# Optimization experiments

Hardware: AMD Instinct MI355X
Metric: run time of the kernel (lower is better)

The kernel has to match this reference:

```python
import jax, jax.numpy as jnp
import numpy as np

N_NODES = 100000
N_EDGES = 3200000
D = 128


def setup_inputs() -> dict:
    key = jax.random.key(0)
    ks = jax.random.split(key, 6)
    x = jax.random.normal(ks[0], (N_NODES, D), dtype=jnp.float32)
    w = jax.random.uniform(ks[1], (N_EDGES,), dtype=jnp.float32)
    W = jax.random.normal(ks[2], (D, D), dtype=jnp.float32) * (1.0 / np.sqrt(D))
    b = jax.random.normal(ks[3], (D,), dtype=jnp.float32) * 0.01
    src = jax.random.randint(ks[4], (N_EDGES,), 0, N_NODES, dtype=jnp.int64)
    dst = jax.random.randint(ks[5], (N_EDGES,), 0, N_NODES, dtype=jnp.int64)
    return {"x": x, "w": w, "W": W, "b": b, "src": src, "dst": dst}


def reference(x, w, W, b, src, dst):
    # h = linear(x)  -> [N, D]
    h = x @ W.T + b
    # u_mul_e: gather source features, scale by per-edge weight  -> [E, D]
    m = h[src] * w[:, None]
    # sum aggregation at destinations (SpMM scatter-add)  -> [N, D]
    out = jax.ops.segment_sum(m, dst, num_segments=N_NODES)
    return out
```

## Files before the change

kernel.cpp:

```cpp
#include <hip/hip_runtime.h>
#include <hip/hip_fp16.h>

constexpr int N_NODES = 100000;
constexpr int N_EDGES = 3200000;
constexpr int NB2 = (N_NODES + 63) >> 6;
constexpr int LCAP = 2432;
constexpr int TILE2 = 12500;
constexpr int NTILE2 = N_EDGES / TILE2;
constexpr int NWIN = 8;
constexpr int NKEY = 64 * NWIN;

__global__ __launch_bounds__(256) void cvt_kernel(const float* __restrict__ x,
                                                  __half* __restrict__ xh) {
  const int stride = gridDim.x * 256;
  const int total = N_NODES * 128 / 4;
  for (int i = blockIdx.x * 256 + threadIdx.x; i < total; i += stride) {
    float4 v = ((const float4*)x)[i];
    ((__half2*)xh)[2 * i] = __floats2half2_rn(v.x, v.y);
    ((__half2*)xh)[2 * i + 1] = __floats2half2_rn(v.z, v.w);
  }
}

__global__ __launch_bounds__(1024) void bin5_kernel(
    const int* __restrict__ src, const int* __restrict__ dst,
    const float* __restrict__ w, int* __restrict__ gtail,
    int2* __restrict__ lists) {
  __shared__ int2 rec[TILE2];
  __shared__ unsigned short lid[TILE2];
  __shared__ int lcnt[NB2];
  __shared__ int loff[NB2];
  __shared__ int lbase[NB2];
  __shared__ int wsum[16];
  const int t = threadIdx.x;
  const int e0 = blockIdx.x * TILE2;

  for (int i = t; i < NB2; i += 1024) lcnt[i] = 0;
  __syncthreads();

  for (int i = t; i < TILE2; i += 1024)
    atomicAdd(&lcnt[dst[e0 + i] >> 6], 1);
  __syncthreads();

  {
    int i0 = 2 * t, i1 = 2 * t + 1;
    int c0 = (i0 < NB2) ? lcnt[i0] : 0;
    int c1 = (i1 < NB2) ? lcnt[i1] : 0;
    int v = c0 + c1;
    int inc = v;
    #pragma unroll
    for (int d = 1; d < 64; d <<= 1) {
      int u = __shfl_up(inc, d, 64);
      if ((t & 63) >= d) inc += u;
    }
    if ((t & 63) == 63) wsum[t >> 6] = inc;
    __syncthreads();
    if (t < 16) {
      int s = wsum[t];
      int inc2 = s;
      #pragma unroll
      for (int d = 1; d < 16; d <<= 1) {
        int u = __shfl_up(inc2, d, 64);
        if (t >= d) inc2 += u;
      }
      wsum[t] = inc2 - s;
    }
    __syncthreads();
    int excl = (inc - v) + wsum[t >> 6];
    if (i0 < NB2) loff[i0] = excl;
    if (i1 < NB2) loff[i1] = excl + c0;
  }
  __syncthreads();

  for (int i = t; i < NB2; i += 1024) {
    int c = lcnt[i];
    lbase[i] = (c > 0) ? atomicAdd(&gtail[i], c) : 0;
  }
  __syncthreads();
  for (int i = t; i < NB2; i += 1024) lcnt[i] = loff[i];
  __syncthreads();

  for (int i = t; i < TILE2; i += 1024) {
    int e = e0 + i;
    int d = dst[e];
    int l = d >> 6;
    int p = atomicAdd(&lcnt[l], 1);
    rec[p] = make_int2(src[e] | ((d & 63) << 17), __float_as_int(w[e]));
    lid[p] = (unsigned short)l;
  }
  __syncthreads();

  for (int q = t; q < TILE2; q += 1024) {
    int l = lid[q];
    int dest = lbase[l] + (q - loff[l]);
    if ((unsigned)dest < (unsigned)LCAP)
      lists[(size_t)l * LCAP + dest] = rec[q];
  }
}

__global__ __launch_bounds__(256) void agg6_kernel(
    const __half* __restrict__ xh, const int2* __restrict__ lists,
    const int* __restrict__ gtail, float* __restrict__ agg_out,
    float* __restrict__ sw) {
  __shared__ int2 sorted[LCAP];
  __shared__ int kcnt[NKEY];
  __shared__ int koff[NKEY + 1];
  __shared__ int kcur[NKEY];
  const int b = blockIdx.x;
  const int t = threadIdx.x;
  const int c = min(gtail[b], LCAP);
  const int2* base = lists + (size_t)b * LCAP;

  for (int i = t; i < NKEY; i += 256) kcnt[i] = 0;
  __syncthreads();

  for (int j = t; j < c; j += 256) {
    int rx = base[j].x;
    int key = ((rx >> 17) & 63) * 8 + ((rx & 0x1FFFF) >> 14);
    atomicAdd(&kcnt[key], 1);
  }
  __syncthreads();

  if (t < 64) {
    int base8 = t * 8;
    int loc[8], run = 0;
    #pragma unroll
    for (int i = 0; i < 8; ++i) { loc[i] = run; run += kcnt[base8 + i]; }
    int inc = run;
    #pragma unroll
    for (int d = 1; d < 64; d <<= 1) {
      int u = __shfl_up(inc, d, 64);
      if (t >= d) inc += u;
    }
    int excl = inc - run;
    #pragma unroll
    for (int i = 0; i < 8; ++i) {
      koff[base8 + i] = excl + loc[i];
      kcur[base8 + i] = excl + loc[i];
    }
    if (t == 63) koff[NKEY] = inc;
  }
  __syncthreads();

  for (int j = t; j < c; j += 256) {
    int2 r = base[j];
    int key = ((r.x >> 17) & 63) * 8 + ((r.x & 0x1FFFF) >> 14);
    int p = atomicAdd(&kcur[key], 1);
    if ((unsigned)p < (unsigned)LCAP) sorted[p] = r;
  }
  __syncthreads();

  const int wv = t >> 6, lane = t & 63;
  const int nd = min(64, N_NODES - b * 64);
  const __half2* xh2 = (const __half2*)xh;
  for (int ri = 0; ri < 16; ++ri) {
    int r = wv * 16 + ri;
    int j0 = min(koff[r * 8], c), j1 = min(koff[r * 8 + 8], c);
    float2 acc = make_float2(0.f, 0.f);
    float sws = 0.f;
    int j = j0;
    for (; j + 8 <= j1; j += 8) {
      int2 e0 = sorted[j];
      int2 e1 = sorted[j + 1];
      int2 e2 = sorted[j + 2];
      int2 e3 = sorted[j + 3];
      int2 e4 = sorted[j + 4];
      int2 e5 = sorted[j + 5];
      int2 e6 = sorted[j + 6];
      int2 e7 = sorted[j + 7];
      float2 v0 = __half22float2(xh2[(size_t)(e0.x & 0x1FFFF) * 64 + lane]);
      float2 v1 = __half22float2(xh2[(size_t)(e1.x & 0x1FFFF) * 64 + lane]);
      float2 v2 = __half22float2(xh2[(size_t)(e2.x & 0x1FFFF) * 64 + lane]);
      float2 v3 = __half22float2(xh2[(size_t)(e3.x & 0x1FFFF) * 64 + lane]);
      float2 v4 = __half22float2(xh2[(size_t)(e4.x & 0x1FFFF) * 64 + lane]);
      float2 v5 = __half22float2(xh2[(size_t)(e5.x & 0x1FFFF) * 64 + lane]);
      float2 v6 = __half22float2(xh2[(size_t)(e6.x & 0x1FFFF) * 64 + lane]);
      float2 v7 = __half22float2(xh2[(size_t)(e7.x & 0x1FFFF) * 64 + lane]);
      float w0 = __int_as_float(e0.y), w1 = __int_as_float(e1.y);
      float w2 = __int_as_float(e2.y), w3 = __int_as_float(e3.y);
      float w4 = __int_as_float(e4.y), w5 = __int_as_float(e5.y);
      float w6 = __int_as_float(e6.y), w7 = __int_as_float(e7.y);
      acc.x = fmaf(w0, v0.x, acc.x); acc.y = fmaf(w0, v0.y, acc.y);
      acc.x = fmaf(w1, v1.x, acc.x); acc.y = fmaf(w1, v1.y, acc.y);
      acc.x = fmaf(w2, v2.x, acc.x); acc.y = fmaf(w2, v2.y, acc.y);
      acc.x = fmaf(w3, v3.x, acc.x); acc.y = fmaf(w3, v3.y, acc.y);
      acc.x = fmaf(w4, v4.x, acc.x); acc.y = fmaf(w4, v4.y, acc.y);
      acc.x = fmaf(w5, v5.x, acc.x); acc.y = fmaf(w5, v5.y, acc.y);
      acc.x = fmaf(w6, v6.x, acc.x); acc.y = fmaf(w6, v6.y, acc.y);
      acc.x = fmaf(w7, v7.x, acc.x); acc.y = fmaf(w7, v7.y, acc.y);
      sws += ((w0 + w1) + (w2 + w3)) + ((w4 + w5) + (w6 + w7));
    }
    for (; j < j1; ++j) {
      int2 e0 = sorted[j];
      float2 v0 = __half22float2(xh2[(size_t)(e0.x & 0x1FFFF) * 64 + lane]);
      float w0 = __int_as_float(e0.y);
      acc.x = fmaf(w0, v0.x, acc.x);
      acc.y = fmaf(w0, v0.y, acc.y);
      sws += w0;
    }
    if (r < nd) {
      ((float2*)agg_out)[(size_t)(b * 64 + r) * 64 + lane] = acc;
      if (lane == 0) sw[b * 64 + r] = sws;
    }
  }
}

__global__ __launch_bounds__(256, 2) void linear3_kernel(
    float* __restrict__ io, const float* __restrict__ W,
    const float* __restrict__ bias, const float* __restrict__ sw) {
  __shared__ float Wt[128][132];
  const int t = threadIdx.x;
  const int row0 = blockIdx.x * 64;

  #pragma unroll
  for (int i = 0; i < 16; ++i) {
    int f4 = t + 256 * i;
    int c = f4 >> 5;
    int k = (f4 & 31) * 4;
    float4 v = *(const float4*)(W + (size_t)c * 128 + k);
    Wt[k + 0][c] = v.x;
    Wt[k + 1][c] = v.y;
    Wt[k + 2][c] = v.z;
    Wt[k + 3][c] = v.w;
  }
  __syncthreads();

  const int tx = t & 15;
  const int ty = t >> 4;
  const float* xr[4];
  #pragma unroll
  for (int i = 0; i < 4; ++i) {
    int r = row0 + ty * 4 + i;
    xr[i] = (r < N_NODES) ? (io + (size_t)r * 128) : io;
  }

  float acc[4][8];
  #pragma unroll
  for (int i = 0; i < 4; ++i)
    #pragma unroll
    for (int j = 0; j < 8; ++j) acc[i][j] = 0.f;

  for (int k0 = 0; k0 < 128; k0 += 4) {
    float4 a[4];
    #pragma unroll
    for (int i = 0; i < 4; ++i) a[i] = *(const float4*)(xr[i] + k0);
    #pragma unroll
    for (int kk = 0; kk < 4; ++kk) {
      int k = k0 + kk;
      float4 b0 = *(const float4*)&Wt[k][tx * 8];
      float4 b1 = *(const float4*)&Wt[k][tx * 8 + 4];
      #pragma unroll
      for (int i = 0; i < 4; ++i) {
        float av = (kk == 0) ? a[i].x : (kk == 1) ? a[i].y
                  : (kk == 2) ? a[i].z : a[i].w;
        acc[i][0] = fmaf(av, b0.x, acc[i][0]);
        acc[i][1] = fmaf(av, b0.y, acc[i][1]);
        acc[i][2] = fmaf(av, b0.z, acc[i][2]);
        acc[i][3] = fmaf(av, b0.w, acc[i][3]);
        acc[i][4] = fmaf(av, b1.x, acc[i][4]);
        acc[i][5] = fmaf(av, b1.y, acc[i][5]);
        acc[i][6] = fmaf(av, b1.z, acc[i][6]);
        acc[i][7] = fmaf(av, b1.w, acc[i][7]);
      }
    }
  }

  float4 bb0 = *(const float4*)(bias + tx * 8);
  float4 bb1 = *(const float4*)(bias + tx * 8 + 4);
  #pragma unroll
  for (int i = 0; i < 4; ++i) {
    int r = row0 + ty * 4 + i;
    if (r < N_NODES) {
      float s = sw[r];
      float4 o0 = make_float4(acc[i][0] + s * bb0.x, acc[i][1] + s * bb0.y,
                              acc[i][2] + s * bb0.z, acc[i][3] + s * bb0.w);
      float4 o1 = make_float4(acc[i][4] + s * bb1.x, acc[i][5] + s * bb1.y,
                              acc[i][6] + s * bb1.z, acc[i][7] + s * bb1.w);
      float* orow = io + (size_t)r * 128 + tx * 8;
      *(float4*)orow = o0;
      *(float4*)(orow + 4) = o1;
    }
  }
}

extern "C" void kernel_launch(void* const* d_in, const int* in_sizes, int n_in,
                              void* d_out, int out_size, void* d_ws, size_t ws_size,
                              hipStream_t stream) {
  const float* x = (const float*)d_in[0];
  const float* w = (const float*)d_in[1];
  const float* W = (const float*)d_in[2];
  const float* bias = (const float*)d_in[3];
  const int* src = (const int*)d_in[4];
  const int* dst = (const int*)d_in[5];
  float* out = (float*)d_out;

  char* p = (char*)d_ws;
  __half* xh = (__half*)p;
  size_t o = (size_t)N_NODES * 128 * sizeof(__half);
  o = (o + 255) & ~(size_t)255;
  int2* lists = (int2*)(p + o);
  o += (size_t)NB2 * LCAP * sizeof(int2);
  int* gtail = (int*)(p + o);
  o += (size_t)NB2 * sizeof(int);
  o = (o + 255) & ~(size_t)255;
  float* sw = (float*)(p + o);

  hipMemsetAsync(gtail, 0, (size_t)NB2 * sizeof(int), stream);
  cvt_kernel<<<2048, 256, 0, stream>>>(x, xh);
  bin5_kernel<<<NTILE2, 1024, 0, stream>>>(src, dst, w, gtail, lists);
  agg6_kernel<<<NB2, 256, 0, stream>>>(xh, lists, gtail, out, sw);
  linear3_kernel<<<NB2, 256, 0, stream>>>(out, W, bias, sw);
}
```

Measured before the change: 390.9 us.

## Make edge binning deterministic via histogram-scan and window-major aggregation order

Splits the binning kernel into a per-tile histogram, a per-bucket prefix scan and a scatter pass, so list offsets come from a scan instead of global atomics. The extra pass re-reads dst and writes count/base arrays. The aggregation kernel now sorts edges window-major (source-range window first, then destination row), so each wave walks source windows in order for better cache locality on gathered features. It accumulates per-row partials in registers and flushes them to LDS on each row change. This adds LDS traffic and branchy flushes in exchange for locality on the random gathers.

```diff
diff --git a/kernel.cpp b/kernel.cpp
--- a/kernel.cpp
+++ b/kernel.cpp
@@ -8,7 +8,7 @@
 constexpr int TILE2 = 12500;
 constexpr int NTILE2 = N_EDGES / TILE2;
 constexpr int NWIN = 8;
-constexpr int NKEY = 64 * NWIN;
+constexpr int NKEY = NWIN * 64;
 
 __global__ __launch_bounds__(256) void cvt_kernel(const float* __restrict__ x,
                                                   __half* __restrict__ xh) {
@@ -21,9 +21,46 @@
   }
 }
 
-__global__ __launch_bounds__(1024) void bin5_kernel(
+__global__ __launch_bounds__(1024) void hist_kernel(const int* __restrict__ dst,
+                                                    int* __restrict__ cnt) {
+  __shared__ int lcnt[NB2];
+  const int t = threadIdx.x;
+  const int e0 = blockIdx.x * TILE2;
+  for (int i = t; i < NB2; i += 1024) lcnt[i] = 0;
+  __syncthreads();
+  for (int i = t; i < TILE2; i += 1024)
+    atomicAdd(&lcnt[dst[e0 + i] >> 6], 1);
+  __syncthreads();
+  for (int i = t; i < NB2; i += 1024) cnt[i * 256 + blockIdx.x] = lcnt[i];
+}
+
+__global__ __launch_bounds__(256) void scan_kernel(const int* __restrict__ cnt,
+                                                   int* __restrict__ bases,
+                                                   int* __restrict__ gtail) {
+  const int wv = threadIdx.x >> 6, lane = threadIdx.x & 63;
+  const int l = blockIdx.x * 4 + wv;
+  if (l >= NB2) return;
+  int4 c4 = ((const int4*)(cnt + (size_t)l * 256))[lane];
+  int sum = ((c4.x + c4.y) + (c4.z + c4.w));
+  int inc = sum;
+  #pragma unroll
+  for (int d = 1; d < 64; d <<= 1) {
+    int u = __shfl_up(inc, d, 64);
+    if (lane >= d) inc += u;
+  }
+  int excl = inc - sum;
+  int4 b4;
+  b4.x = excl;
+  b4.y = excl + c4.x;
+  b4.z = excl + c4.x + c4.y;
+  b4.w = excl + c4.x + c4.y + c4.z;
+  ((int4*)(bases + (size_t)l * 256))[lane] = b4;
+  if (lane == 63) gtail[l] = inc;
+}
+
+__global__ __launch_bounds__(1024) void scatter_kernel(
     const int* __restrict__ src, const int* __restrict__ dst,
-    const float* __restrict__ w, int* __restrict__ gtail,
+    const float* __restrict__ w, const int* __restrict__ bases,
     int2* __restrict__ lists) {
   __shared__ int2 rec[TILE2];
   __shared__ unsigned short lid[TILE2];
@@ -71,10 +108,7 @@
   }
   __syncthreads();
 
-  for (int i = t; i < NB2; i += 1024) {
-    int c = lcnt[i];
-    lbase[i] = (c > 0) ? atomicAdd(&gtail[i], c) : 0;
-  }
+  for (int i = t; i < NB2; i += 1024) lbase[i] = bases[(size_t)i * 256 + blockIdx.x];
   __syncthreads();
   for (int i = t; i < NB2; i += 1024) lcnt[i] = loff[i];
   __syncthreads();
@@ -97,11 +131,13 @@
   }
 }
 
-__global__ __launch_bounds__(256) void agg6_kernel(
+__global__ __launch_bounds__(256) void agg7_kernel(
     const __half* __restrict__ xh, const int2* __restrict__ lists,
     const int* __restrict__ gtail, float* __restrict__ agg_out,
     float* __restrict__ sw) {
   __shared__ int2 sorted[LCAP];
+  __shared__ float acc_lds[4][16][128];
+  __shared__ float swl[64];
   __shared__ int kcnt[NKEY];
   __shared__ int koff[NKEY + 1];
   __shared__ int kcur[NKEY];
@@ -111,11 +147,13 @@
   const int2* base = lists + (size_t)b * LCAP;
 
   for (int i = t; i < NKEY; i += 256) kcnt[i] = 0;
+  for (int i = t; i < 4 * 16 * 128; i += 256) ((float*)acc_lds)[i] = 0.f;
+  if (t < 64) swl[t] = 0.f;
   __syncthreads();
 
   for (int j = t; j < c; j += 256) {
     int rx = base[j].x;
-    int key = ((rx >> 17) & 63) * 8 + ((rx & 0x1FFFF) >> 14);
+    int key = ((rx & 0x1FFFF) >> 14) * 64 + ((rx >> 17) & 63);
     atomicAdd(&kcnt[key], 1);
   }
   __syncthreads();
@@ -143,7 +181,7 @@
 
   for (int j = t; j < c; j += 256) {
     int2 r = base[j];
-    int key = ((r.x >> 17) & 63) * 8 + ((r.x & 0x1FFFF) >> 14);
+    int key = ((r.x & 0x1FFFF) >> 14) * 64 + ((r.x >> 17) & 63);
     int p = atomicAdd(&kcur[key], 1);
     if ((unsigned)p < (unsigned)LCAP) sorted[p] = r;
   }
@@ -152,54 +190,61 @@
   const int wv = t >> 6, lane = t & 63;
   const int nd = min(64, N_NODES - b * 64);
   const __half2* xh2 = (const __half2*)xh;
-  for (int ri = 0; ri < 16; ++ri) {
-    int r = wv * 16 + ri;
-    int j0 = min(koff[r * 8], c), j1 = min(koff[r * 8 + 8], c);
-    float2 acc = make_float2(0.f, 0.f);
-    float sws = 0.f;
+  float2 racc = make_float2(0.f, 0.f);
+  float rsws = 0.f;
+  int cur = -1;
+
+#define FLUSH()                                              \
+  if (cur >= 0) {                                            \
+    int rl_ = cur & 15;                                      \
+    acc_lds[wv][rl_][lane] += racc.x;                        \
+    acc_lds[wv][rl_][64 + lane] += racc.y;                   \
+    if (lane == 0) swl[(wv << 4) + rl_] += rsws;             \
+    racc.x = 0.f; racc.y = 0.f; rsws = 0.f;                  \
+  }
+
+  for (int s = 0; s < NWIN; ++s) {
+    int j0 = min(koff[s * 64 + (wv << 4)], c);
+    int j1 = min(koff[s * 64 + (wv << 4) + 16], c);
     int j = j0;
     for (; j + 8 <= j1; j += 8) {
-      int2 e0 = sorted[j];
-      int2 e1 = sorted[j + 1];
-      int2 e2 = sorted[j + 2];
-      int2 e3 = sorted[j + 3];
-      int2 e4 = sorted[j + 4];
-      int2 e5 = sorted[j + 5];
-      int2 e6 = sorted[j + 6];
-      int2 e7 = sorted[j + 7];
-      float2 v0 = __half22float2(xh2[(size_t)(e0.x & 0x1FFFF) * 64 + lane]);
-      float2 v1 = __half22float2(xh2[(size_t)(e1.x & 0x1FFFF) * 64 + lane]);
-      float2 v2 = __half22float2(xh2[(size_t)(e2.x & 0x1FFFF) * 64 + lane]);
-      float2 v3 = __half22float2(xh2[(size_t)(e3.x & 0x1FFFF) * 64 + lane]);
-      float2 v4 = __half22float2(xh2[(size_t)(e4.x & 0x1FFFF) * 64 + lane]);
-      float2 v5 = __half22float2(xh2[(size_t)(e5.x & 0x1FFFF) * 64 + lane]);
-      float2 v6 = __half22float2(xh2[(size_t)(e6.x & 0x1FFFF) * 64 + lane]);
-      float2 v7 = __half22float2(xh2[(size_t)(e7.x & 0x1FFFF) * 64 + lane]);
-      float w0 = __int_as_float(e0.y), w1 = __int_as_float(e1.y);
-      float w2 = __int_as_float(e2.y), w3 = __int_as_float(e3.y);
-      float w4 = __int_as_float(e4.y), w5 = __int_as_float(e5.y);
-      float w6 = __int_as_float(e6.y), w7 = __int_as_float(e7.y);
-      acc.x = fmaf(w0, v0.x, acc.x); acc.y = fmaf(w0, v0.y, acc.y);
-      acc.x = fmaf(w1, v1.x, acc.x); acc.y = fmaf(w1, v1.y, acc.y);
-      acc.x = fmaf(w2, v2.x, acc.x); acc.y = fmaf(w2, v2.y, acc.y);
-      acc.x = fmaf(w3, v3.x, acc.x); acc.y = fmaf(w3, v3.y, acc.y);
-      acc.x = fmaf(w4, v4.x, acc.x); acc.y = fmaf(w4, v4.y, acc.y);
-      acc.x = fmaf(w5, v5.x, acc.x); acc.y = fmaf(w5, v5.y, acc.y);
-      acc.x = fmaf(w6, v6.x, acc.x); acc.y = fmaf(w6, v6.y, acc.y);
-      acc.x = fmaf(w7, v7.x, acc.x); acc.y = fmaf(w7, v7.y, acc.y);
-      sws += ((w0 + w1) + (w2 + w3)) + ((w4 + w5) + (w6 + w7));
+      int2 e[8];
+      float2 v[8];
+      #pragma unroll
+      for (int i = 0; i < 8; ++i) e[i] = sorted[j + i];
+      #pragma unroll
+      for (int i = 0; i < 8; ++i)
+        v[i] = __half22float2(xh2[(size_t)(e[i].x & 0x1FFFF) * 64 + lane]);
+      #pragma unroll
+      for (int i = 0; i < 8; ++i) {
+        int row = (e[i].x >> 17) & 63;
+        if (row != cur) { FLUSH(); cur = row; }
+        float wt = __int_as_float(e[i].y);
+        racc.x = fmaf(wt, v[i].x, racc.x);
+        racc.y = fmaf(wt, v[i].y, racc.y);
+        rsws += wt;
+      }
     }
     for (; j < j1; ++j) {
       int2 e0 = sorted[j];
       float2 v0 = __half22float2(xh2[(size_t)(e0.x & 0x1FFFF) * 64 + lane]);
-      float w0 = __int_as_float(e0.y);
-      acc.x = fmaf(w0, v0.x, acc.x);
-      acc.y = fmaf(w0, v0.y, acc.y);
-      sws += w0;
-    }
+      int row = (e0.x >> 17) & 63;
+      if (row != cur) { FLUSH(); cur = row; }
+      float wt = __int_as_float(e0.y);
+      racc.x = fmaf(wt, v0.x, racc.x);
+      racc.y = fmaf(wt, v0.y, racc.y);
+      rsws += wt;
+    }
+  }
+  FLUSH();
+#undef FLUSH
+
+  for (int ri = 0; ri < 16; ++ri) {
+    int r = (wv << 4) + ri;
     if (r < nd) {
-      ((float2*)agg_out)[(size_t)(b * 64 + r) * 64 + lane] = acc;
-      if (lane == 0) sw[b * 64 + r] = sws;
+      float2 o = make_float2(acc_lds[wv][ri][lane], acc_lds[wv][ri][64 + lane]);
+      ((float2*)agg_out)[(size_t)(b * 64 + r) * 64 + lane] = o;
+      if (lane == 0) sw[b * 64 + r] = swl[r];
     }
   }
 }
@@ -299,14 +344,22 @@
   o = (o + 255) & ~(size_t)255;
   int2* lists = (int2*)(p + o);
   o += (size_t)NB2 * LCAP * sizeof(int2);
+  o = (o + 255) & ~(size_t)255;
+  int* cnt = (int*)(p + o);
+  o += (size_t)NB2 * 256 * sizeof(int);
+  o = (o + 255) & ~(size_t)255;
+  int* bases = (int*)(p + o);
+  o += (size_t)NB2 * 256 * sizeof(int);
+  o = (o + 255) & ~(size_t)255;
   int* gtail = (int*)(p + o);
   o += (size_t)NB2 * sizeof(int);
   o = (o + 255) & ~(size_t)255;
   float* sw = (float*)(p + o);
 
-  hipMemsetAsync(gtail, 0, (size_t)NB2 * sizeof(int), stream);
   cvt_kernel<<<2048, 256, 0, stream>>>(x, xh);
-  bin5_kernel<<<NTILE2, 1024, 0, stream>>>(src, dst, w, gtail, lists);
-  agg6_kernel<<<NB2, 256, 0, stream>>>(xh, lists, gtail, out, sw);
+  hist_kernel<<<NTILE2, 1024, 0, stream>>>(dst, cnt);
+  scan_kernel<<<(NB2 + 3) / 4, 256, 0, stream>>>(cnt, bases, gtail);
+  scatter_kernel<<<NTILE2, 1024, 0, stream>>>(src, dst, w, bases, lists);
+  agg7_kernel<<<NB2, 256, 0, stream>>>(xh, lists, gtail, out, sw);
   linear3_kernel<<<NB2, 256, 0, stream>>>(out, W, bias, sw);
 }
```

Result: slower. 492.8 us (+26.1%).
